# Optimization experiments

Hardware: AMD Instinct MI355X
Metric: run time of the kernel (lower is better)

The kernel has to match this reference:

```python
import jax, jax.numpy as jnp
import numpy as np

B, S, D, H = 2, 4096, 128, 128
EPS = 1e-6
NEG_INF = -1e30


def _complex_linear(xr, xi, Wr, Wi, br, bi):
    # x: (B,S,D); W: (H,D); complex linear (Wr + i Wi)(xr + i xi) + (br + i bi) per layer math:
    # real_out = (xr Wr + br) - (xi Wi + bi); imag_out = (xi Wr + br) + (xr Wi + bi)
    out_r = xr @ Wr.T + br - (xi @ Wi.T + bi)
    out_i = xi @ Wr.T + br + (xr @ Wi.T + bi)
    return out_r, out_i


def setup_inputs() -> dict:
    key = jax.random.key(0)
    ks = jax.random.split(key, 24)
    scale = 1.0 / np.sqrt(D)
    def W(k):
        return jax.random.normal(k, (H, D), jnp.float32) * scale
    def b(k):
        return jax.random.normal(k, (H,), jnp.float32) * 0.01
    inp = {
        "Z_q": jax.random.normal(ks[0], (B, 2, S, D, 1), jnp.float32),
        "Z_k": jax.random.normal(ks[1], (B, 2, S, D, 1), jnp.float32),
        "Z_v": jax.random.normal(ks[2], (B, 2, S, D, 1), jnp.float32),
        "Wq_r": W(ks[3]), "Wq_i": W(ks[4]), "bq_r": b(ks[5]), "bq_i": b(ks[6]),
        "Wk_r": W(ks[7]), "Wk_i": W(ks[8]), "bk_r": b(ks[9]), "bk_i": b(ks[10]),
        "Wv_r": W(ks[11]), "Wv_i": W(ks[12]), "bv_r": b(ks[13]), "bv_i": b(ks[14]),
        "Wp_r": W(ks[15]), "Wp_i": W(ks[16]), "bp_r": b(ks[17]), "bp_i": b(ks[18]),
        "noise_floor": jnp.asarray(1.0, jnp.float32),
        "tau": jnp.asarray(0.0, jnp.float32),
    }
    return inp


def reference(Z_q, Z_k, Z_v,
              Wq_r, Wq_i, bq_r, bq_i,
              Wk_r, Wk_i, bk_r, bk_i,
              Wv_r, Wv_i, bv_r, bv_i,
              Wp_r, Wp_i, bp_r, bp_i,
              noise_floor, tau):
    # squeeze trailing singleton; split real/imag -> (B,S,D)
    zqr, zqi = Z_q[:, 0, :, :, 0], Z_q[:, 1, :, :, 0]
    zkr, zki = Z_k[:, 0, :, :, 0], Z_k[:, 1, :, :, 0]
    zvr, zvi = Z_v[:, 0, :, :, 0], Z_v[:, 1, :, :, 0]

    Qr, Qi = _complex_linear(zqr, zqi, Wq_r, Wq_i, bq_r, bq_i)
    Kr, Ki = _complex_linear(zkr, zki, Wk_r, Wk_i, bk_r, bk_i)
    Vr, Vi = _complex_linear(zvr, zvi, Wv_r, Wv_i, bv_r, bv_i)

    # InverseMahalanobis: R2[b,i,j] = sum_h |Q[b,i]-K[b,j]|^2
    q2 = jnp.sum(Qr * Qr + Qi * Qi, axis=-1)          # (B,S)
    k2 = jnp.sum(Kr * Kr + Ki * Ki, axis=-1)          # (B,S)
    re_qk = (jnp.einsum('bsh,bth->bst', Qr, Kr)
             + jnp.einsum('bsh,bth->bst', Qi, Ki))    # (B,S,S)
    R2 = q2[:, :, None] + k2[:, None, :] - 2.0 * re_qk

    attn_scores = -jax.nn.softplus(tau) * jnp.log(noise_floor ** 2 + R2 + EPS)
    mask = jnp.tril(jnp.ones((S, S), dtype=bool))[None]
    attn_scores = jnp.where(mask, attn_scores, NEG_INF)
    attn_weights = jax.nn.softmax(attn_scores / jnp.sqrt(jnp.float32(H)), axis=-1)

    # attn (real) times complex V
    est_r = jnp.einsum('bst,bth->bsh', attn_weights, Vr)
    est_i = jnp.einsum('bst,bth->bsh', attn_weights, Vi)

    out_r, out_i = _complex_linear(est_r, est_i, Wp_r, Wp_i, bp_r, bp_i)
    out = jnp.stack((out_r, out_i), axis=1)[..., None]  # (B,2,S,H,1)
    return out, attn_weights
```

## Files before the change

### kernel.cpp

```cpp
#include <hip/hip_runtime.h>

#define S_LEN 4096
#define NBATCH 2
#define ROWS (NBATCH*S_LEN)
#define OUT_ELEMS 2097152

typedef _Float16 f16;
typedef _Float16 f16x8 __attribute__((ext_vector_type(8)));
typedef _Float16 f16x4 __attribute__((ext_vector_type(4)));
typedef float f32x4 __attribute__((ext_vector_type(4)));

#define MT_OFF    0x000000
#define BIAS_OFF  0x080000
#define SC_OFF    0x081000
#define QH_OFF    0x100000
#define KH_OFF    0x500000
#define VT_OFF    0x900000
#define Q2_OFF    0xD00000
#define K2_OFF    0xD10000
#define L_OFF     0xD20000
#define RS_OFF    0xE00000
#define EST_OFF   0x1200000
#define PW_OFF    0x9200000
#define WS_NEED   0xD200000

#define MFMA16(A,B,C) __builtin_amdgcn_mfma_f32_16x16x32_f16(A,B,C,0,0,0)

__device__ __forceinline__ void async_cp16(f16* lds, const f16* g) {
  __builtin_amdgcn_global_load_lds(
      (const __attribute__((address_space(1))) void*)g,
      (__attribute__((address_space(3))) void*)lds, 16, 0, 0);
}

template<int TR>
__device__ __forceinline__ void stage16(f16* lds, const f16* g, int stride, int tid) {
#pragma unroll
  for (int i = 0; i < TR/64; ++i) {
    int idx = i*256 + tid;
    int row = idx >> 2;
    int c = (idx & 3) ^ ((row >> 1) & 3);
    async_cp16(lds + idx*8, g + (size_t)row*stride + c*8);
  }
}

template<int TR>
__device__ __forceinline__ void stage32(f16* lds, const float* g, int stride, int tid,
                                        const float* rowscale) {
#pragma unroll
  for (int i = 0; i < TR/32; ++i) {
    int idx = i*256 + tid;
    int row = idx >> 3, c = idx & 7;
    const float4* gp = (const float4*)(g + (size_t)row*stride + c*4);
    float4 v = *gp;
    float sc = rowscale ? rowscale[row] : 1.0f;
    f16x4 h; h[0]=(f16)(v.x*sc); h[1]=(f16)(v.y*sc); h[2]=(f16)(v.z*sc); h[3]=(f16)(v.w*sc);
    int slot = (((c >> 1) ^ ((row >> 1) & 3)) << 3) + (c & 1)*4;
    *(f16x4*)(lds + row*32 + slot) = h;
  }
}

template<int MI, int NJ>
__device__ __forceinline__ void mfma_step(const f16* Asm, const f16* Bsm, int lane,
                                          int wm, int wn, f32x4 (&acc)[MI][NJ]) {
  f16x8 a[MI], b[NJ];
  int rr = lane & 15, kc = lane >> 4;
#pragma unroll
  for (int i=0;i<MI;i++) {
    int m = wm + i*16 + rr;
    a[i] = *(const f16x8*)(Asm + m*32 + ((kc ^ ((m>>1)&3)) << 3));
  }
#pragma unroll
  for (int j=0;j<NJ;j++) {
    int n = wn + j*16 + rr;
    b[j] = *(const f16x8*)(Bsm + n*32 + ((kc ^ ((n>>1)&3)) << 3));
  }
#pragma unroll
  for (int i=0;i<MI;i++)
#pragma unroll
    for (int j=0;j<NJ;j++) acc[i][j] = MFMA16(a[i], b[j], acc[i][j]);
}

__global__ __launch_bounds__(256)
void k_build(const float* Wqr, const float* Wqi, const float* bqr, const float* bqi,
             const float* Wkr, const float* Wki, const float* bkr, const float* bki,
             const float* Wvr, const float* Wvi, const float* bvr, const float* bvi,
             const float* Wpr, const float* Wpi, const float* bpr, const float* bpi,
             f16* Mt, float* bias) {
  int mat = blockIdx.x;
  const float *Wr, *Wi, *br, *bi;
  if (mat == 0)      { Wr=Wqr; Wi=Wqi; br=bqr; bi=bqi; }
  else if (mat == 1) { Wr=Wkr; Wi=Wki; br=bkr; bi=bki; }
  else if (mat == 2) { Wr=Wvr; Wi=Wvi; br=bvr; bi=bvi; }
  else               { Wr=Wpr; Wi=Wpi; br=bpr; bi=bpi; }
  int idx = blockIdx.y*256 + threadIdx.x;
  int n = idx >> 8, k = idx & 255;
  int d = k & 127, h = n & 127;
  float w = (k < 128) ? ((n < 128) ? Wr[h*128+d] : Wi[h*128+d])
                      : ((n < 128) ? -Wi[h*128+d] : Wr[h*128+d]);
  Mt[mat*65536 + n*256 + k] = (f16)w;
  if (k == 0)
    bias[mat*256 + n] = (n < 128) ? (br[n] - bi[n]) : (br[n-128] + bi[n-128]);
}

__global__ __launch_bounds__(256)
void k_init(float* zreg, float* sc, const float* nf, const float* tau) {
  int idx = blockIdx.x*256 + threadIdx.x;
  if (idx < 12288) ((float4*)zreg)[idx] = make_float4(0.f,0.f,0.f,0.f);
  if (idx == 0) {
    float t = tau[0];
    float c = __builtin_log2f(1.0f + __builtin_exp2f(t * 1.4426950408889634f))
              * 0.6931471805599453f;
    sc[0] = -c * 0.08838834764831845f;
    sc[1] = nf[0]*nf[0] + 1e-6f;
  }
}

__global__ __launch_bounds__(256)
void k_proj(const float* Zq, const float* Zk, const float* Zv,
            const f16* Mt, const float* bias,
            f16* Qh, f16* Kh, f16* Vt, float* q2, float* k2) {
  __shared__ f16 Asm[64*32];
  __shared__ f16 Bsm[128*32];
  __shared__ float bias_s[128];
  int tid = threadIdx.x;
  int mode = blockIdx.z;
  int m0 = blockIdx.x * 64, n0 = blockIdx.y * 128;
  const float* Z = (mode==0) ? Zq : (mode==1 ? Zk : Zv);
  const f16* Bt = Mt + mode*65536;
  if (tid < 128) bias_s[tid] = bias[mode*256 + n0 + tid];
  int b = m0 >> 12, s0 = m0 & 4095;
  int lane = tid & 63, w = tid >> 6;
  int wm = (w >> 1)*32, wn = (w & 1)*64;
  f32x4 acc[2][4] = {};
  for (int kb = 0; kb < 8; ++kb) {
    int k0 = kb*32;
    int part = k0 >> 7, d0 = k0 & 127;
    const float* Ag = Z + (((size_t)(b*2 + part))*S_LEN + s0)*128 + d0;
    stage32<64>(Asm, Ag, 128, tid, nullptr);
    stage16<128>(Bsm, Bt + n0*256 + k0, 256, tid);
    __syncthreads();
    mfma_step<2,4>(Asm, Bsm, lane, wm, wn, acc);
    __syncthreads();
  }
  int rr = (lane>>4)*4, cc = lane & 15;
  if (mode < 2) {
    f16* O = (mode==0) ? Qh : Kh;
    float rs[2][4];
#pragma unroll
    for (int i=0;i<2;i++)
#pragma unroll
      for (int r=0;r<4;r++) rs[i][r]=0.f;
#pragma unroll
    for (int i=0;i<2;i++)
#pragma unroll
      for (int j=0;j<4;j++) {
        int cl = wn + j*16 + cc;
        int cg = n0 + cl;
        float bv = bias_s[cl];
#pragma unroll
        for (int r=0;r<4;r++) {
          int rg = m0 + wm + i*16 + rr + r;
          f16 hv = (f16)(acc[i][j][r] + bv);
          O[(size_t)rg*256 + cg] = hv;
          float fv = (float)hv;
          rs[i][r] += fv*fv;
        }
      }
#pragma unroll
    for (int m=8;m>=1;m>>=1)
#pragma unroll
      for (int i=0;i<2;i++)
#pragma unroll
        for (int r=0;r<4;r++) rs[i][r] += __shfl_xor(rs[i][r], m, 64);
    if (cc == 0) {
      float* T = (mode==0) ? q2 : k2;
#pragma unroll
      for (int i=0;i<2;i++)
#pragma unroll
        for (int r=0;r<4;r++) {
          int rg = m0 + wm + i*16 + rr + r;
          atomicAdd(&T[rg], rs[i][r]);
        }
    }
  } else {
#pragma unroll
    for (int i=0;i<2;i++) {
      int t0 = s0 + wm + i*16 + rr;
#pragma unroll
      for (int j=0;j<4;j++) {
        int cl = wn + j*16 + cc;
        int cg = n0 + cl;
        float bv = bias_s[cl];
        f16x4 h4;
#pragma unroll
        for (int r=0;r<4;r++) h4[r] = (f16)(acc[i][j][r] + bv);
        *(f16x4*)(Vt + (size_t)b*1048576 + (size_t)cg*4096 + t0) = h4;
      }
    }
  }
}

__global__ __launch_bounds__(256)
void k_attn(const f16* Qh, const f16* Kh, const float* q2, const float* k2,
            const float* sc, float* rsum, f16* Pws) {
  __shared__ f16 Asm[128*32];
  __shared__ f16 Bsm[128*32];
  __shared__ float q2s[128], k2s[128];
  int x = blockIdx.x;
  int b = x / 528, r = x % 528;
  int sb = (int)((__builtin_sqrtf(8.f*(float)r + 1.f) - 1.f)*0.5f);
  while ((sb+1)*(sb+2)/2 <= r) sb++;
  while (sb*(sb+1)/2 > r) sb--;
  int tb = r - sb*(sb+1)/2;
  int s0 = sb*128, t0 = tb*128;
  int tid = threadIdx.x;
  if (tid < 128) {
    q2s[tid] = q2[b*S_LEN + s0 + tid];
    k2s[tid] = k2[b*S_LEN + t0 + tid];
  }
  float kc = sc[0], nf2 = sc[1];
  int lane = tid & 63, w = tid >> 6;
  int wm = (w >> 1)*64, wn = (w & 1)*64;
  const f16* Ag = Qh + ((size_t)(b*S_LEN) + s0)*256;
  const f16* Bg = Kh + ((size_t)(b*S_LEN) + t0)*256;
  f32x4 acc[4][4] = {};
  for (int kb=0;kb<8;kb++) {
    stage16<128>(Asm, Ag + kb*32, 256, tid);
    stage16<128>(Bsm, Bg + kb*32, 256, tid);
    __syncthreads();
    mfma_step<4,4>(Asm, Bsm, lane, wm, wn, acc);
    __syncthreads();
  }
  int rr = (lane>>4)*4, cc = lane & 15;
  bool diag = (tb == sb);
  float rs[4][4];
#pragma unroll
  for (int i=0;i<4;i++)
#pragma unroll
    for (int rg=0;rg<4;rg++) rs[i][rg]=0.f;
#pragma unroll
  for (int i=0;i<4;i++)
#pragma unroll
    for (int j=0;j<4;j++) {
      int cl = wn + j*16 + cc;
      float kv = k2s[cl];
#pragma unroll
      for (int rg=0;rg<4;rg++) {
        int rl = wm + i*16 + rr + rg;
        float xx = nf2 + q2s[rl] + kv - 2.0f*acc[i][j][rg];
        float P = __builtin_exp2f(kc * __builtin_log2f(__builtin_fmaxf(xx, 1e-6f)));
        if (diag && (t0+cl) > (s0+rl)) P = 0.f;
        Pws[((size_t)(b*S_LEN) + s0 + rl)*S_LEN + t0 + cl] = (f16)P;
        rs[i][rg] += P;
      }
    }
#pragma unroll
  for (int m=8;m>=1;m>>=1)
#pragma unroll
    for (int i=0;i<4;i++)
#pragma unroll
      for (int rg=0;rg<4;rg++) rs[i][rg] += __shfl_xor(rs[i][rg], m, 64);
  if (cc == 0) {
    float* R = rsum + ((size_t)((b*32+sb)*32+tb))*256 + (wn>>6)*128;
#pragma unroll
    for (int i=0;i<4;i++)
#pragma unroll
      for (int rg=0;rg<4;rg++)
        R[wm + i*16 + rr + rg] = rs[i][rg];
  }
}

__global__ __launch_bounds__(256)
void k_lred(const float* rsum, float* lsum) {
  int s = blockIdx.x*256 + threadIdx.x;
  int b = s >> 12, srow = s & 4095;
  int sb = srow >> 7, rowin = srow & 127;
  const float* R = rsum + ((size_t)((b*32+sb)*32))*256 + rowin;
  float acc = 0.f;
  for (int tb = 0; tb <= sb; ++tb) acc += R[tb*256] + R[tb*256+128];
  lsum[s] = acc;
}

__global__ __launch_bounds__(256)
void k_pv(const f16* Pws, const f16* Vt, float* est) {
  __shared__ f16 Asm[128*32];
  __shared__ f16 Bsm[128*32];
  int r = blockIdx.x;
  int nb = blockIdx.y, b = blockIdx.z;
  int sb = 0;
  while (r >= ((sb>>1)+1)) { r -= (sb>>1)+1; sb++; }
  int c = r;
  int s0 = sb*128, h0 = nb*128;
  int tid = threadIdx.x;
  int lane = tid & 63, w = tid >> 6;
  int wm = (w>>1)*64, wn = (w&1)*64;
  int tb0 = c*2, tb1 = tb0 + 2; if (tb1 > sb+1) tb1 = sb+1;
  const f16* Abase = Pws + ((size_t)(b*S_LEN) + s0)*S_LEN;
  const f16* Bbase = Vt + (size_t)b*1048576 + (size_t)h0*4096;
  f32x4 acc[4][4] = {};
  for (int tb = tb0; tb < tb1; ++tb)
    for (int kk = 0; kk < 4; ++kk) {
      int t0 = tb*128 + kk*32;
      stage16<128>(Asm, Abase + t0, S_LEN, tid);
      stage16<128>(Bsm, Bbase + t0, 4096, tid);
      __syncthreads();
      mfma_step<4,4>(Asm, Bsm, lane, wm, wn, acc);
      __syncthreads();
    }
  float* E = est + (size_t)c*2097152;
  int rr = (lane>>4)*4, cc = lane & 15;
#pragma unroll
  for (int i=0;i<4;i++)
#pragma unroll
    for (int j=0;j<4;j++) {
      int cg = h0 + wn + j*16 + cc;
#pragma unroll
      for (int rg=0;rg<4;rg++) {
        int rgl = s0 + wm + i*16 + rr + rg;
        E[((size_t)(b*S_LEN) + rgl)*256 + cg] = acc[i][j][rg];
      }
    }
}

__global__ __launch_bounds__(256)
void k_norm(const f16* __restrict__ Pws, const float* __restrict__ lsum,
            float* __restrict__ attn) {
  int base = blockIdx.x*1024 + threadIdx.x;
#pragma unroll
  for (int u = 0; u < 4; ++u) {
    int lin = base + u*256;
    int row = lin >> 10, t4 = lin & 1023;
    int srow = row & 4095;
    int t0 = t4 << 2;
    float4 o = make_float4(0.f,0.f,0.f,0.f);
    if (t0 <= srow) {
      float invl = 1.0f / lsum[row];
      f16x4 p = *(const f16x4*)(Pws + ((size_t)row<<12) + t0);
      o.x = (float)p[0]*invl;
      o.y = (t0+1 <= srow) ? (float)p[1]*invl : 0.f;
      o.z = (t0+2 <= srow) ? (float)p[2]*invl : 0.f;
      o.w = (t0+3 <= srow) ? (float)p[3]*invl : 0.f;
    }
    ((float4*)attn)[lin] = o;
  }
}

__global__ __launch_bounds__(256)
void k_out(const float* est, const f16* Mt, const float* bias, const float* lsum,
           float* outp) {
  __shared__ f16 Asm[16*32];
  __shared__ f16 Bsm[256*32];
  __shared__ float bias_s[256];
  __shared__ float ls[16];
  int m0 = blockIdx.x*16;
  int tid = threadIdx.x;
  int b = m0 >> 12, s0 = m0 & 4095;
  int sb = s0 >> 7, nch = (sb>>1) + 1;
  if (tid < 256) bias_s[tid] = bias[3*256 + tid];
  if (tid < 16)  ls[tid] = 1.0f / lsum[b*S_LEN + s0 + tid];
  __syncthreads();
  int lane = tid & 63, w = tid >> 6;
  int wn = w*64;
  const f16* Bt = Mt + 3*65536;
  f32x4 acc[1][4] = {};
  for (int kb=0;kb<8;kb++) {
    if (tid < 128) {
      int row = tid >> 3, c4 = tid & 7;
      const float* basep = est + ((size_t)(b*S_LEN) + s0 + row)*256 + kb*32 + c4*4;
      float4 v = make_float4(0.f,0.f,0.f,0.f);
      for (int ch = 0; ch < nch; ++ch) {
        float4 q = *(const float4*)(basep + (size_t)ch*2097152);
        v.x += q.x; v.y += q.y; v.z += q.z; v.w += q.w;
      }
      float scl = ls[row];
      f16x4 h; h[0]=(f16)(v.x*scl); h[1]=(f16)(v.y*scl); h[2]=(f16)(v.z*scl); h[3]=(f16)(v.w*scl);
      int slot = (((c4 >> 1) ^ ((row >> 1) & 3)) << 3) + (c4 & 1)*4;
      *(f16x4*)(Asm + row*32 + slot) = h;
    }
    stage16<256>(Bsm, Bt + kb*32, 256, tid);
    __syncthreads();
    mfma_step<1,4>(Asm, Bsm, lane, 0, wn, acc);
    __syncthreads();
  }
  int rr = (lane>>4)*4, cc = lane & 15;
#pragma unroll
  for (int j=0;j<4;j++) {
    int cg = wn + j*16 + cc;
    int comp = cg >> 7, h = cg & 127;
    float bv = bias_s[cg];
#pragma unroll
    for (int rg=0;rg<4;rg++) {
      int s = s0 + rr + rg;
      outp[(((size_t)(b*2 + comp))*S_LEN + s)*128 + h] = acc[0][j][rg] + bv;
    }
  }
}

extern "C" void kernel_launch(void* const* d_in, const int* in_sizes, int n_in,
                              void* d_out, int out_size, void* d_ws, size_t ws_size,
                              hipStream_t stream) {
  (void)in_sizes; (void)n_in; (void)out_size;
  if (ws_size < (size_t)WS_NEED) return;
  const float* Zq = (const float*)d_in[0];
  const float* Zk = (const float*)d_in[1];
  const float* Zv = (const float*)d_in[2];
  char* ws = (char*)d_ws;
  f16*   Mt   = (f16*)(ws + MT_OFF);
  float* bias = (float*)(ws + BIAS_OFF);
  float* sc   = (float*)(ws + SC_OFF);
  f16*   Qh   = (f16*)(ws + QH_OFF);
  f16*   Kh   = (f16*)(ws + KH_OFF);
  f16*   Vt   = (f16*)(ws + VT_OFF);
  float* q2   = (float*)(ws + Q2_OFF);
  float* k2   = (float*)(ws + K2_OFF);
  float* lsum = (float*)(ws + L_OFF);
  float* rsum = (float*)(ws + RS_OFF);
  float* est  = (float*)(ws + EST_OFF);
  f16*   Pws  = (f16*)(ws + PW_OFF);
  float* outp = (float*)d_out;
  float* attn = outp + OUT_ELEMS;

  k_build<<<dim3(4,256), 256, 0, stream>>>(
      (const float*)d_in[3],  (const float*)d_in[4],  (const float*)d_in[5],  (const float*)d_in[6],
      (const float*)d_in[7],  (const float*)d_in[8],  (const float*)d_in[9],  (const float*)d_in[10],
      (const float*)d_in[11], (const float*)d_in[12], (const float*)d_in[13], (const float*)d_in[14],
      (const float*)d_in[15], (const float*)d_in[16], (const float*)d_in[17], (const float*)d_in[18],
      Mt, bias);
  k_init<<<48, 256, 0, stream>>>(q2, sc, (const float*)d_in[19], (const float*)d_in[20]);
  k_proj<<<dim3(128,2,3), 256, 0, stream>>>(Zq, Zk, Zv, Mt, bias, Qh, Kh, Vt, q2, k2);
  k_attn<<<1056, 256, 0, stream>>>(Qh, Kh, q2, k2, sc, rsum, Pws);
  k_lred<<<32, 256, 0, stream>>>(rsum, lsum);
  k_pv<<<dim3(272,2,2), 256, 0, stream>>>(Pws, Vt, est);
  k_norm<<<8192, 256, 0, stream>>>(Pws, lsum, attn);
  k_out<<<512, 256, 0, stream>>>(est, Mt, bias, lsum, outp);
}
```

Before: 355.4 us.

## Fuse pipeline into persistent megakernel with grid barriers and balanced PV split

Replaces the separate projection, attention, row-sum, PV, normalization and output kernels with one persistent 512-block kernel that moves between phases through software grid barriers. PV work is redistributed into four balanced splits per row-block pair with partial outputs zeroed up front. Atomics for q2/k2 are replaced with partial sums written per slice. This removes launch gaps and load imbalance, but relies on all 512 blocks being co-resident for the barrier, and the normalize and output phases now share the grid.

```diff
diff --git a/kernel.cpp b/kernel.cpp
--- a/kernel.cpp
+++ b/kernel.cpp
@@ -4,6 +4,7 @@
 #define NBATCH 2
 #define ROWS (NBATCH*S_LEN)
 #define OUT_ELEMS 2097152
+#define NBLK 512
 
 typedef _Float16 f16;
 typedef _Float16 f16x8 __attribute__((ext_vector_type(8)));
@@ -13,16 +14,17 @@
 #define MT_OFF    0x000000
 #define BIAS_OFF  0x080000
 #define SC_OFF    0x081000
+#define BAR_OFF   0x082000
 #define QH_OFF    0x100000
 #define KH_OFF    0x500000
 #define VT_OFF    0x900000
-#define Q2_OFF    0xD00000
-#define K2_OFF    0xD10000
-#define L_OFF     0xD20000
+#define Q2P_OFF   0xD00000
+#define K2P_OFF   0xD20000
+#define LS_OFF    0xD40000
 #define RS_OFF    0xE00000
-#define EST_OFF   0x1200000
-#define PW_OFF    0x9200000
-#define WS_NEED   0xD200000
+#define ESTP_OFF  0x1200000
+#define PW_OFF    0x3200000
+#define WS_NEED   0x7200000
 
 #define MFMA16(A,B,C) __builtin_amdgcn_mfma_f32_16x16x32_f16(A,B,C,0,0,0)
 
@@ -44,16 +46,14 @@
 }
 
 template<int TR>
-__device__ __forceinline__ void stage32(f16* lds, const float* g, int stride, int tid,
-                                        const float* rowscale) {
+__device__ __forceinline__ void stage32(f16* lds, const float* g, int stride, int tid) {
 #pragma unroll
   for (int i = 0; i < TR/32; ++i) {
     int idx = i*256 + tid;
     int row = idx >> 3, c = idx & 7;
     const float4* gp = (const float4*)(g + (size_t)row*stride + c*4);
     float4 v = *gp;
-    float sc = rowscale ? rowscale[row] : 1.0f;
-    f16x4 h; h[0]=(f16)(v.x*sc); h[1]=(f16)(v.y*sc); h[2]=(f16)(v.z*sc); h[3]=(f16)(v.w*sc);
+    f16x4 h; h[0]=(f16)v.x; h[1]=(f16)v.y; h[2]=(f16)v.z; h[3]=(f16)v.w;
     int slot = (((c >> 1) ^ ((row >> 1) & 3)) << 3) + (c & 1)*4;
     *(f16x4*)(lds + row*32 + slot) = h;
   }
@@ -80,318 +80,355 @@
     for (int j=0;j<NJ;j++) acc[i][j] = MFMA16(a[i], b[j], acc[i][j]);
 }
 
+__device__ __forceinline__ void gbar(int* bar) {
+  __syncthreads();
+  if (threadIdx.x == 0) {
+    __threadfence();
+    int gen = __hip_atomic_load(&bar[1], __ATOMIC_RELAXED, __HIP_MEMORY_SCOPE_AGENT);
+    int old = __hip_atomic_fetch_add(&bar[0], 1, __ATOMIC_ACQ_REL, __HIP_MEMORY_SCOPE_AGENT);
+    if (old == NBLK-1) {
+      __hip_atomic_store(&bar[0], 0, __ATOMIC_RELAXED, __HIP_MEMORY_SCOPE_AGENT);
+      __hip_atomic_fetch_add(&bar[1], 1, __ATOMIC_RELEASE, __HIP_MEMORY_SCOPE_AGENT);
+    } else {
+      while (__hip_atomic_load(&bar[1], __ATOMIC_ACQUIRE, __HIP_MEMORY_SCOPE_AGENT) == gen)
+        __builtin_amdgcn_s_sleep(2);
+    }
+    __threadfence();
+  }
+  __syncthreads();
+}
+
 __global__ __launch_bounds__(256)
-void k_build(const float* Wqr, const float* Wqi, const float* bqr, const float* bqi,
-             const float* Wkr, const float* Wki, const float* bkr, const float* bki,
-             const float* Wvr, const float* Wvi, const float* bvr, const float* bvi,
-             const float* Wpr, const float* Wpi, const float* bpr, const float* bpi,
-             f16* Mt, float* bias) {
-  int mat = blockIdx.x;
-  const float *Wr, *Wi, *br, *bi;
-  if (mat == 0)      { Wr=Wqr; Wi=Wqi; br=bqr; bi=bqi; }
-  else if (mat == 1) { Wr=Wkr; Wi=Wki; br=bkr; bi=bki; }
-  else if (mat == 2) { Wr=Wvr; Wi=Wvi; br=bvr; bi=bvi; }
-  else               { Wr=Wpr; Wi=Wpi; br=bpr; bi=bpi; }
-  int idx = blockIdx.y*256 + threadIdx.x;
-  int n = idx >> 8, k = idx & 255;
-  int d = k & 127, h = n & 127;
-  float w = (k < 128) ? ((n < 128) ? Wr[h*128+d] : Wi[h*128+d])
-                      : ((n < 128) ? -Wi[h*128+d] : Wr[h*128+d]);
-  Mt[mat*65536 + n*256 + k] = (f16)w;
-  if (k == 0)
-    bias[mat*256 + n] = (n < 128) ? (br[n] - bi[n]) : (br[n-128] + bi[n-128]);
-}
-
-__global__ __launch_bounds__(256)
-void k_init(float* zreg, float* sc, const float* nf, const float* tau) {
+void k_init(const float* Wqr, const float* Wqi, const float* bqr, const float* bqi,
+            const float* Wkr, const float* Wki, const float* bkr, const float* bki,
+            const float* Wvr, const float* Wvi, const float* bvr, const float* bvi,
+            const float* Wpr, const float* Wpi, const float* bpr, const float* bpi,
+            f16* Mt, float* bias, float* sc, float* estp, int* bar,
+            const float* nf, const float* tau) {
   int idx = blockIdx.x*256 + threadIdx.x;
-  if (idx < 12288) ((float4*)zreg)[idx] = make_float4(0.f,0.f,0.f,0.f);
+  if (idx < 262144) {
+    int mat = idx >> 16, rest = idx & 65535;
+    int n = rest >> 8, k = rest & 255;
+    const float *Wr, *Wi, *br, *bi;
+    if (mat == 0)      { Wr=Wqr; Wi=Wqi; br=bqr; bi=bqi; }
+    else if (mat == 1) { Wr=Wkr; Wi=Wki; br=bkr; bi=bki; }
+    else if (mat == 2) { Wr=Wvr; Wi=Wvi; br=bvr; bi=bvi; }
+    else               { Wr=Wpr; Wi=Wpi; br=bpr; bi=bpi; }
+    int d = k & 127, h = n & 127;
+    float w = (k < 128) ? ((n < 128) ? Wr[h*128+d] : Wi[h*128+d])
+                        : ((n < 128) ? -Wi[h*128+d] : Wr[h*128+d]);
+    Mt[mat*65536 + n*256 + k] = (f16)w;
+    if (k == 0)
+      bias[mat*256 + n] = (n < 128) ? (br[n] - bi[n]) : (br[n-128] + bi[n-128]);
+  }
+  float4 z = make_float4(0.f,0.f,0.f,0.f);
+#pragma unroll
+  for (int u = 0; u < 4; ++u)
+    ((float4*)estp)[idx + u*524288] = z;
   if (idx == 0) {
     float t = tau[0];
     float c = __builtin_log2f(1.0f + __builtin_exp2f(t * 1.4426950408889634f))
               * 0.6931471805599453f;
     sc[0] = -c * 0.08838834764831845f;
     sc[1] = nf[0]*nf[0] + 1e-6f;
-  }
-}
-
-__global__ __launch_bounds__(256)
-void k_proj(const float* Zq, const float* Zk, const float* Zv,
-            const f16* Mt, const float* bias,
-            f16* Qh, f16* Kh, f16* Vt, float* q2, float* k2) {
-  __shared__ f16 Asm[64*32];
-  __shared__ f16 Bsm[128*32];
-  __shared__ float bias_s[128];
-  int tid = threadIdx.x;
-  int mode = blockIdx.z;
-  int m0 = blockIdx.x * 64, n0 = blockIdx.y * 128;
-  const float* Z = (mode==0) ? Zq : (mode==1 ? Zk : Zv);
-  const f16* Bt = Mt + mode*65536;
-  if (tid < 128) bias_s[tid] = bias[mode*256 + n0 + tid];
-  int b = m0 >> 12, s0 = m0 & 4095;
+    bar[0] = 0; bar[1] = 0;
+  }
+}
+
+__global__ __launch_bounds__(256, 2)
+void k_mega(const float* Zq, const float* Zk, const float* Zv,
+            const f16* Mt, const float* bias, const float* sc,
+            f16* Qh, f16* Kh, f16* Vt, float* q2p, float* k2p,
+            float* rsum, float* lsum, float* estp, f16* Pws,
+            float* attn, float* outp, int* bar) {
+  __shared__ __align__(16) char smem[18496];
+  int bid = blockIdx.x, tid = threadIdx.x;
   int lane = tid & 63, w = tid >> 6;
-  int wm = (w >> 1)*32, wn = (w & 1)*64;
-  f32x4 acc[2][4] = {};
-  for (int kb = 0; kb < 8; ++kb) {
-    int k0 = kb*32;
-    int part = k0 >> 7, d0 = k0 & 127;
-    const float* Ag = Z + (((size_t)(b*2 + part))*S_LEN + s0)*128 + d0;
-    stage32<64>(Asm, Ag, 128, tid, nullptr);
-    stage16<128>(Bsm, Bt + n0*256 + k0, 256, tid);
+  int rr = (lane>>4)*4, cc = lane & 15;
+
+  for (int job = bid; job < 768; job += NBLK) {
+    f16* Asm = (f16*)smem;
+    f16* Bsm = (f16*)(smem + 4096);
+    float* bias_s = (float*)(smem + 12288);
+    int mode = job >> 8, rem = job & 255;
+    int m0 = (rem >> 1)*64, n0 = (rem & 1)*128;
+    const float* Z = (mode==0) ? Zq : (mode==1 ? Zk : Zv);
+    const f16* Bt = Mt + mode*65536;
+    if (tid < 128) bias_s[tid] = bias[mode*256 + n0 + tid];
+    int b = m0 >> 12, s0 = m0 & 4095;
+    int wm = (w >> 1)*32, wn = (w & 1)*64;
+    f32x4 acc[2][4] = {};
+    for (int kb = 0; kb < 8; ++kb) {
+      int k0 = kb*32;
+      int part = k0 >> 7, d0 = k0 & 127;
+      const float* Ag = Z + (((size_t)(b*2 + part))*S_LEN + s0)*128 + d0;
+      stage32<64>(Asm, Ag, 128, tid);
+      stage16<128>(Bsm, Bt + n0*256 + k0, 256, tid);
+      __syncthreads();
+      mfma_step<2,4>(Asm, Bsm, lane, wm, wn, acc);
+      __syncthreads();
+    }
+    if (mode < 2) {
+      f16* O = (mode==0) ? Qh : Kh;
+      float rs[2][4];
+#pragma unroll
+      for (int i=0;i<2;i++)
+#pragma unroll
+        for (int r=0;r<4;r++) rs[i][r]=0.f;
+#pragma unroll
+      for (int i=0;i<2;i++)
+#pragma unroll
+        for (int j=0;j<4;j++) {
+          int cl = wn + j*16 + cc;
+          float bv = bias_s[cl];
+#pragma unroll
+          for (int r=0;r<4;r++) {
+            int rg = m0 + wm + i*16 + rr + r;
+            f16 hv = (f16)(acc[i][j][r] + bv);
+            O[(size_t)rg*256 + n0 + cl] = hv;
+            float fv = (float)hv;
+            rs[i][r] += fv*fv;
+          }
+        }
+#pragma unroll
+      for (int m=8;m>=1;m>>=1)
+#pragma unroll
+        for (int i=0;i<2;i++)
+#pragma unroll
+          for (int r=0;r<4;r++) rs[i][r] += __shfl_xor(rs[i][r], m, 64);
+      if (cc == 0) {
+        float* T = ((mode==0) ? q2p : k2p) + ((n0>>7)*2 + (wn>>6))*8192;
+#pragma unroll
+        for (int i=0;i<2;i++)
+#pragma unroll
+          for (int r=0;r<4;r++)
+            T[m0 + wm + i*16 + rr + r] = rs[i][r];
+      }
+    } else {
+#pragma unroll
+      for (int i=0;i<2;i++) {
+        int t0 = s0 + wm + i*16 + rr;
+#pragma unroll
+        for (int j=0;j<4;j++) {
+          int cl = wn + j*16 + cc;
+          float bv = bias_s[cl];
+          f16x4 h4;
+#pragma unroll
+          for (int r=0;r<4;r++) h4[r] = (f16)(acc[i][j][r] + bv);
+          *(f16x4*)(Vt + (size_t)b*1048576 + (size_t)(n0+cl)*4096 + t0) = h4;
+        }
+      }
+    }
     __syncthreads();
-    mfma_step<2,4>(Asm, Bsm, lane, wm, wn, acc);
-    __syncthreads();
-  }
-  int rr = (lane>>4)*4, cc = lane & 15;
-  if (mode < 2) {
-    f16* O = (mode==0) ? Qh : Kh;
-    float rs[2][4];
-#pragma unroll
-    for (int i=0;i<2;i++)
-#pragma unroll
-      for (int r=0;r<4;r++) rs[i][r]=0.f;
-#pragma unroll
-    for (int i=0;i<2;i++)
+  }
+  gbar(bar);
+
+  for (int job = bid; job < 1056; job += NBLK) {
+    f16* Asm = (f16*)smem;
+    f16* Bsm = (f16*)(smem + 8192);
+    float* q2s = (float*)(smem + 16384);
+    float* k2s = (float*)(smem + 16896);
+    int b = job / 528, r = job % 528;
+    int sb = (int)((__builtin_sqrtf(8.f*(float)r + 1.f) - 1.f)*0.5f);
+    while ((sb+1)*(sb+2)/2 <= r) sb++;
+    while (sb*(sb+1)/2 > r) sb--;
+    int tb = r - sb*(sb+1)/2;
+    int s0 = sb*128, t0 = tb*128;
+    if (tid < 128) {
+      int rq = b*S_LEN + s0 + tid, rk = b*S_LEN + t0 + tid;
+      q2s[tid] = q2p[rq] + q2p[8192+rq] + q2p[16384+rq] + q2p[24576+rq];
+      k2s[tid] = k2p[rk] + k2p[8192+rk] + k2p[16384+rk] + k2p[24576+rk];
+    }
+    float kcs = sc[0], nf2 = sc[1];
+    int wm = (w >> 1)*64, wn = (w & 1)*64;
+    const f16* Ag = Qh + ((size_t)(b*S_LEN) + s0)*256;
+    const f16* Bg = Kh + ((size_t)(b*S_LEN) + t0)*256;
+    f32x4 acc[4][4] = {};
+    for (int kb=0;kb<8;kb++) {
+      stage16<128>(Asm, Ag + kb*32, 256, tid);
+      stage16<128>(Bsm, Bg + kb*32, 256, tid);
+      __syncthreads();
+      mfma_step<4,4>(Asm, Bsm, lane, wm, wn, acc);
+      __syncthreads();
+    }
+    bool diag = (tb == sb);
+    float rs[4][4];
+#pragma unroll
+    for (int i=0;i<4;i++)
+#pragma unroll
+      for (int rg=0;rg<4;rg++) rs[i][rg]=0.f;
+#pragma unroll
+    for (int i=0;i<4;i++)
 #pragma unroll
       for (int j=0;j<4;j++) {
         int cl = wn + j*16 + cc;
-        int cg = n0 + cl;
-        float bv = bias_s[cl];
-#pragma unroll
-        for (int r=0;r<4;r++) {
-          int rg = m0 + wm + i*16 + rr + r;
-          f16 hv = (f16)(acc[i][j][r] + bv);
-          O[(size_t)rg*256 + cg] = hv;
-          float fv = (float)hv;
-          rs[i][r] += fv*fv;
+        float kv = k2s[cl];
+#pragma unroll
+        for (int rg=0;rg<4;rg++) {
+          int rl = wm + i*16 + rr + rg;
+          float xx = nf2 + q2s[rl] + kv - 2.0f*acc[i][j][rg];
+          float P = __builtin_exp2f(kcs * __builtin_log2f(__builtin_fmaxf(xx, 1e-6f)));
+          if (diag && (t0+cl) > (s0+rl)) P = 0.f;
+          Pws[((size_t)(b*S_LEN) + s0 + rl)*S_LEN + t0 + cl] = (f16)P;
+          rs[i][rg] += P;
         }
       }
 #pragma unroll
     for (int m=8;m>=1;m>>=1)
 #pragma unroll
-      for (int i=0;i<2;i++)
-#pragma unroll
-        for (int r=0;r<4;r++) rs[i][r] += __shfl_xor(rs[i][r], m, 64);
+      for (int i=0;i<4;i++)
+#pragma unroll
+        for (int rg=0;rg<4;rg++) rs[i][rg] += __shfl_xor(rs[i][rg], m, 64);
     if (cc == 0) {
-      float* T = (mode==0) ? q2 : k2;
-#pragma unroll
-      for (int i=0;i<2;i++)
-#pragma unroll
-        for (int r=0;r<4;r++) {
-          int rg = m0 + wm + i*16 + rr + r;
-          atomicAdd(&T[rg], rs[i][r]);
-        }
+      float* R = rsum + ((size_t)((b*32+sb)*32+tb))*256 + (wn>>6)*128;
+#pragma unroll
+      for (int i=0;i<4;i++)
+#pragma unroll
+        for (int rg=0;rg<4;rg++)
+          R[wm + i*16 + rr + rg] = rs[i][rg];
+    }
+    __syncthreads();
+  }
+  gbar(bar);
+
+  if (bid < 256) {
+    f16* Asm = (f16*)smem;
+    f16* Bsm = (f16*)(smem + 8192);
+    int j = bid;
+    int p = j & 15, spl = (j>>4)&3, nbh = (j>>6)&1, b = j>>7;
+    int h0 = nbh*128;
+    int wm = (w>>1)*64, wn = (w&1)*64;
+    int st = (33*spl + 3) >> 2;
+    int en = (33*spl + 36) >> 2;
+    const f16* Bbase = Vt + (size_t)b*1048576 + (size_t)h0*4096;
+    f32x4 acc[4][4] = {};
+    int currow = -1;
+    for (int idx = st; idx < en; ++idx) {
+      int row = (idx <= p) ? p : 31-p;
+      int tb  = (idx <= p) ? idx : idx - (p+1);
+      if (row != currow) {
+        if (currow >= 0) {
+          float* E = estp + (size_t)spl*2097152 + ((size_t)(b*S_LEN) + currow*128)*256;
+#pragma unroll
+          for (int i=0;i<4;i++)
+#pragma unroll
+            for (int j2=0;j2<4;j2++)
+#pragma unroll
+              for (int rg=0;rg<4;rg++) {
+                E[(size_t)(wm + i*16 + rr + rg)*256 + h0 + wn + j2*16 + cc] = acc[i][j2][rg];
+                acc[i][j2][rg] = 0.f;
+              }
+        }
+        currow = row;
+      }
+      const f16* Abase = Pws + ((size_t)(b*S_LEN) + row*128)*S_LEN;
+      for (int kk=0;kk<4;kk++) {
+        int t0 = tb*128 + kk*32;
+        stage16<128>(Asm, Abase + t0, S_LEN, tid);
+        stage16<128>(Bsm, Bbase + t0, 4096, tid);
+        __syncthreads();
+        mfma_step<4,4>(Asm, Bsm, lane, wm, wn, acc);
+        __syncthreads();
+      }
+    }
+    {
+      float* E = estp + (size_t)spl*2097152 + ((size_t)(b*S_LEN) + currow*128)*256;
+#pragma unroll
+      for (int i=0;i<4;i++)
+#pragma unroll
+        for (int j2=0;j2<4;j2++)
+#pragma unroll
+          for (int rg=0;rg<4;rg++)
+            E[(size_t)(wm + i*16 + rr + rg)*256 + h0 + wn + j2*16 + cc] = acc[i][j2][rg];
     }
   } else {
-#pragma unroll
-    for (int i=0;i<2;i++) {
-      int t0 = s0 + wm + i*16 + rr;
-#pragma unroll
-      for (int j=0;j<4;j++) {
-        int cl = wn + j*16 + cc;
-        int cg = n0 + cl;
-        float bv = bias_s[cl];
-        f16x4 h4;
-#pragma unroll
-        for (int r=0;r<4;r++) h4[r] = (f16)(acc[i][j][r] + bv);
-        *(f16x4*)(Vt + (size_t)b*1048576 + (size_t)cg*4096 + t0) = h4;
-      }
-    }
-  }
-}
-
-__global__ __launch_bounds__(256)
-void k_attn(const f16* Qh, const f16* Kh, const float* q2, const float* k2,
-            const float* sc, float* rsum, f16* Pws) {
-  __shared__ f16 Asm[128*32];
-  __shared__ f16 Bsm[128*32];
-  __shared__ float q2s[128], k2s[128];
-  int x = blockIdx.x;
-  int b = x / 528, r = x % 528;
-  int sb = (int)((__builtin_sqrtf(8.f*(float)r + 1.f) - 1.f)*0.5f);
-  while ((sb+1)*(sb+2)/2 <= r) sb++;
-  while (sb*(sb+1)/2 > r) sb--;
-  int tb = r - sb*(sb+1)/2;
-  int s0 = sb*128, t0 = tb*128;
-  int tid = threadIdx.x;
-  if (tid < 128) {
-    q2s[tid] = q2[b*S_LEN + s0 + tid];
-    k2s[tid] = k2[b*S_LEN + t0 + tid];
-  }
-  float kc = sc[0], nf2 = sc[1];
-  int lane = tid & 63, w = tid >> 6;
-  int wm = (w >> 1)*64, wn = (w & 1)*64;
-  const f16* Ag = Qh + ((size_t)(b*S_LEN) + s0)*256;
-  const f16* Bg = Kh + ((size_t)(b*S_LEN) + t0)*256;
-  f32x4 acc[4][4] = {};
-  for (int kb=0;kb<8;kb++) {
-    stage16<128>(Asm, Ag + kb*32, 256, tid);
-    stage16<128>(Bsm, Bg + kb*32, 256, tid);
+    float* part = (float*)smem;
+    float* lss  = (float*)(smem + 1024);
+    int nb2 = bid - 256;
+    {
+      int r2 = tid >> 3, j8 = tid & 7;
+      int rowg = nb2*32 + r2;
+      int b = rowg >> 12, srow = rowg & 4095;
+      int sb = srow >> 7, rowin = srow & 127;
+      const float* R = rsum + ((size_t)((b*32+sb)*32))*256 + rowin;
+      float s = 0.f;
+      for (int tb = j8; tb <= sb; tb += 8) s += R[tb*256] + R[tb*256+128];
+      part[tid] = s;
+    }
     __syncthreads();
-    mfma_step<4,4>(Asm, Bsm, lane, wm, wn, acc);
+    if (tid < 32) {
+      float s = 0.f;
+#pragma unroll
+      for (int u=0;u<8;u++) s += part[tid*8+u];
+      lss[tid] = s;
+      lsum[nb2*32 + tid] = s;
+    }
     __syncthreads();
-  }
-  int rr = (lane>>4)*4, cc = lane & 15;
-  bool diag = (tb == sb);
-  float rs[4][4];
-#pragma unroll
-  for (int i=0;i<4;i++)
-#pragma unroll
-    for (int rg=0;rg<4;rg++) rs[i][rg]=0.f;
-#pragma unroll
-  for (int i=0;i<4;i++)
+    for (int r2 = 0; r2 < 32; ++r2) {
+      int rowg = nb2*32 + r2;
+      int srow = rowg & 4095;
+      float invl = 1.0f / lss[r2];
+      const f16* src = Pws + (size_t)rowg*S_LEN;
+      float4* dst = (float4*)(attn + (size_t)rowg*S_LEN);
+      for (int q = tid; q < 1024; q += 256) {
+        int t0 = q*4;
+        float4 o = make_float4(0.f,0.f,0.f,0.f);
+        if (t0 <= srow) {
+          f16x4 pv4 = *(const f16x4*)(src + t0);
+          o.x = (float)pv4[0]*invl;
+          o.y = (t0+1 <= srow) ? (float)pv4[1]*invl : 0.f;
+          o.z = (t0+2 <= srow) ? (float)pv4[2]*invl : 0.f;
+          o.w = (t0+3 <= srow) ? (float)pv4[3]*invl : 0.f;
+        }
+        dst[q] = o;
+      }
+    }
+  }
+  gbar(bar);
+
+  {
+    f16* Asm = (f16*)smem;
+    f16* Bsm = (f16*)(smem + 1024);
+    float* bias_s = (float*)(smem + 1024 + 16384);
+    float* ls = (float*)(smem + 1024 + 16384 + 1024);
+    int m0 = bid*16;
+    int b = m0 >> 12, s0 = m0 & 4095;
+    bias_s[tid] = bias[3*256 + tid];
+    if (tid < 16) ls[tid] = 1.0f / lsum[b*S_LEN + s0 + tid];
+    __syncthreads();
+    int wn = w*64;
+    const f16* Bt = Mt + 3*65536;
+    f32x4 acc[1][4] = {};
+    for (int kb=0;kb<8;kb++) {
+      if (tid < 128) {
+        int row = tid >> 3, c4 = tid & 7;
+        const float* basep = estp + ((size_t)(b*S_LEN) + s0 + row)*256 + kb*32 + c4*4;
+        float4 v = make_float4(0.f,0.f,0.f,0.f);
+#pragma unroll
+        for (int ch = 0; ch < 4; ++ch) {
+          float4 q = *(const float4*)(basep + (size_t)ch*2097152);
+          v.x += q.x; v.y += q.y; v.z += q.z; v.w += q.w;
+        }
+        float scl = ls[row];
+        f16x4 h; h[0]=(f16)(v.x*scl); h[1]=(f16)(v.y*scl); h[2]=(f16)(v.z*scl); h[3]=(f16)(v.w*scl);
+        int slot = (((c4 >> 1) ^ ((row >> 1) & 3)) << 3) + (c4 & 1)*4;
+        *(f16x4*)(Asm + row*32 + slot) = h;
+      }
+      stage16<256>(Bsm, Bt + kb*32, 256, tid);
+      __syncthreads();
+      mfma_step<1,4>(Asm, Bsm, lane, 0, wn, acc);
+      __syncthreads();
+    }
 #pragma unroll
     for (int j=0;j<4;j++) {
-      int cl = wn + j*16 + cc;
-      float kv = k2s[cl];
+      int cg = wn + j*16 + cc;
+      int comp = cg >> 7, h = cg & 127;
+      float bv = bias_s[cg];
 #pragma unroll
       for (int rg=0;rg<4;rg++) {
-        int rl = wm + i*16 + rr + rg;
-        float xx = nf2 + q2s[rl] + kv - 2.0f*acc[i][j][rg];
-        float P = __builtin_exp2f(kc * __builtin_log2f(__builtin_fmaxf(xx, 1e-6f)));
-        if (diag && (t0+cl) > (s0+rl)) P = 0.f;
-        Pws[((size_t)(b*S_LEN) + s0 + rl)*S_LEN + t0 + cl] = (f16)P;
-        rs[i][rg] += P;
-      }
-    }
-#pragma unroll
-  for (int m=8;m>=1;m>>=1)
-#pragma unroll
-    for (int i=0;i<4;i++)
-#pragma unroll
-      for (int rg=0;rg<4;rg++) rs[i][rg] += __shfl_xor(rs[i][rg], m, 64);
-  if (cc == 0) {
-    float* R = rsum + ((size_t)((b*32+sb)*32+tb))*256 + (wn>>6)*128;
-#pragma unroll
-    for (int i=0;i<4;i++)
-#pragma unroll
-      for (int rg=0;rg<4;rg++)
-        R[wm + i*16 + rr + rg] = rs[i][rg];
-  }
-}
-
-__global__ __launch_bounds__(256)
-void k_lred(const float* rsum, float* lsum) {
-  int s = blockIdx.x*256 + threadIdx.x;
-  int b = s >> 12, srow = s & 4095;
-  int sb = srow >> 7, rowin = srow & 127;
-  const float* R = rsum + ((size_t)((b*32+sb)*32))*256 + rowin;
-  float acc = 0.f;
-  for (int tb = 0; tb <= sb; ++tb) acc += R[tb*256] + R[tb*256+128];
-  lsum[s] = acc;
-}
-
-__global__ __launch_bounds__(256)
-void k_pv(const f16* Pws, const f16* Vt, float* est) {
-  __shared__ f16 Asm[128*32];
-  __shared__ f16 Bsm[128*32];
-  int r = blockIdx.x;
-  int nb = blockIdx.y, b = blockIdx.z;
-  int sb = 0;
-  while (r >= ((sb>>1)+1)) { r -= (sb>>1)+1; sb++; }
-  int c = r;
-  int s0 = sb*128, h0 = nb*128;
-  int tid = threadIdx.x;
-  int lane = tid & 63, w = tid >> 6;
-  int wm = (w>>1)*64, wn = (w&1)*64;
-  int tb0 = c*2, tb1 = tb0 + 2; if (tb1 > sb+1) tb1 = sb+1;
-  const f16* Abase = Pws + ((size_t)(b*S_LEN) + s0)*S_LEN;
-  const f16* Bbase = Vt + (size_t)b*1048576 + (size_t)h0*4096;
-  f32x4 acc[4][4] = {};
-  for (int tb = tb0; tb < tb1; ++tb)
-    for (int kk = 0; kk < 4; ++kk) {
-      int t0 = tb*128 + kk*32;
-      stage16<128>(Asm, Abase + t0, S_LEN, tid);
-      stage16<128>(Bsm, Bbase + t0, 4096, tid);
-      __syncthreads();
-      mfma_step<4,4>(Asm, Bsm, lane, wm, wn, acc);
-      __syncthreads();
-    }
-  float* E = est + (size_t)c*2097152;
-  int rr = (lane>>4)*4, cc = lane & 15;
-#pragma unroll
-  for (int i=0;i<4;i++)
-#pragma unroll
-    for (int j=0;j<4;j++) {
-      int cg = h0 + wn + j*16 + cc;
-#pragma unroll
-      for (int rg=0;rg<4;rg++) {
-        int rgl = s0 + wm + i*16 + rr + rg;
-        E[((size_t)(b*S_LEN) + rgl)*256 + cg] = acc[i][j][rg];
-      }
-    }
-}
-
-__global__ __launch_bounds__(256)
-void k_norm(const f16* __restrict__ Pws, const float* __restrict__ lsum,
-            float* __restrict__ attn) {
-  int base = blockIdx.x*1024 + threadIdx.x;
-#pragma unroll
-  for (int u = 0; u < 4; ++u) {
-    int lin = base + u*256;
-    int row = lin >> 10, t4 = lin & 1023;
-    int srow = row & 4095;
-    int t0 = t4 << 2;
-    float4 o = make_float4(0.f,0.f,0.f,0.f);
-    if (t0 <= srow) {
-      float invl = 1.0f / lsum[row];
-      f16x4 p = *(const f16x4*)(Pws + ((size_t)row<<12) + t0);
-      o.x = (float)p[0]*invl;
-      o.y = (t0+1 <= srow) ? (float)p[1]*invl : 0.f;
-      o.z = (t0+2 <= srow) ? (float)p[2]*invl : 0.f;
-      o.w = (t0+3 <= srow) ? (float)p[3]*invl : 0.f;
-    }
-    ((float4*)attn)[lin] = o;
-  }
-}
-
-__global__ __launch_bounds__(256)
-void k_out(const float* est, const f16* Mt, const float* bias, const float* lsum,
-           float* outp) {
-  __shared__ f16 Asm[16*32];
-  __shared__ f16 Bsm[256*32];
-  __shared__ float bias_s[256];
-  __shared__ float ls[16];
-  int m0 = blockIdx.x*16;
-  int tid = threadIdx.x;
-  int b = m0 >> 12, s0 = m0 & 4095;
-  int sb = s0 >> 7, nch = (sb>>1) + 1;
-  if (tid < 256) bias_s[tid] = bias[3*256 + tid];
-  if (tid < 16)  ls[tid] = 1.0f / lsum[b*S_LEN + s0 + tid];
-  __syncthreads();
-  int lane = tid & 63, w = tid >> 6;
-  int wn = w*64;
-  const f16* Bt = Mt + 3*65536;
-  f32x4 acc[1][4] = {};
-  for (int kb=0;kb<8;kb++) {
-    if (tid < 128) {
-      int row = tid >> 3, c4 = tid & 7;
-      const float* basep = est + ((size_t)(b*S_LEN) + s0 + row)*256 + kb*32 + c4*4;
-      float4 v = make_float4(0.f,0.f,0.f,0.f);
-      for (int ch = 0; ch < nch; ++ch) {
-        float4 q = *(const float4*)(basep + (size_t)ch*2097152);
-        v.x += q.x; v.y += q.y; v.z += q.z; v.w += q.w;
-      }
-      float scl = ls[row];
-      f16x4 h; h[0]=(f16)(v.x*scl); h[1]=(f16)(v.y*scl); h[2]=(f16)(v.z*scl); h[3]=(f16)(v.w*scl);
-      int slot = (((c4 >> 1) ^ ((row >> 1) & 3)) << 3) + (c4 & 1)*4;
-      *(f16x4*)(Asm + row*32 + slot) = h;
-    }
-    stage16<256>(Bsm, Bt + kb*32, 256, tid);
-    __syncthreads();
-    mfma_step<1,4>(Asm, Bsm, lane, 0, wn, acc);
-    __syncthreads();
-  }
-  int rr = (lane>>4)*4, cc = lane & 15;
-#pragma unroll
-  for (int j=0;j<4;j++) {
-    int cg = wn + j*16 + cc;
-    int comp = cg >> 7, h = cg & 127;
-    float bv = bias_s[cg];
-#pragma unroll
-    for (int rg=0;rg<4;rg++) {
-      int s = s0 + rr + rg;
-      outp[(((size_t)(b*2 + comp))*S_LEN + s)*128 + h] = acc[0][j][rg] + bv;
+        int s = s0 + rr + rg;
+        outp[(((size_t)(b*2 + comp))*S_LEN + s)*128 + h] = acc[0][j][rg] + bv;
+      }
     }
   }
 }
@@ -401,36 +438,30 @@
                               hipStream_t stream) {
   (void)in_sizes; (void)n_in; (void)out_size;
   if (ws_size < (size_t)WS_NEED) return;
-  const float* Zq = (const float*)d_in[0];
-  const float* Zk = (const float*)d_in[1];
-  const float* Zv = (const float*)d_in[2];
   char* ws = (char*)d_ws;
   f16*   Mt   = (f16*)(ws + MT_OFF);
   float* bias = (float*)(ws + BIAS_OFF);
   float* sc   = (float*)(ws + SC_OFF);
+  int*   bar  = (int*)(ws + BAR_OFF);
   f16*   Qh   = (f16*)(ws + QH_OFF);
   f16*   Kh   = (f16*)(ws + KH_OFF);
   f16*   Vt   = (f16*)(ws + VT_OFF);
-  float* q2   = (float*)(ws + Q2_OFF);
-  float* k2   = (float*)(ws + K2_OFF);
-  float* lsum = (float*)(ws + L_OFF);
+  float* q2p  = (float*)(ws + Q2P_OFF);
+  float* k2p  = (float*)(ws + K2P_OFF);
+  float* lsum = (float*)(ws + LS_OFF);
   float* rsum = (float*)(ws + RS_OFF);
-  float* est  = (float*)(ws + EST_OFF);
+  float* estp = (float*)(ws + ESTP_OFF);
   f16*   Pws  = (f16*)(ws + PW_OFF);
   float* outp = (float*)d_out;
   float* attn = outp + OUT_ELEMS;
 
-  k_build<<<dim3(4,256), 256, 0, stream>>>(
+  k_init<<<2048, 256, 0, stream>>>(
       (const float*)d_in[3],  (const float*)d_in[4],  (const float*)d_in[5],  (const float*)d_in[6],
       (const float*)d_in[7],  (const float*)d_in[8],  (const float*)d_in[9],  (const float*)d_in[10],
       (const float*)d_in[11], (const float*)d_in[12], (const float*)d_in[13], (const float*)d_in[14],
       (const float*)d_in[15], (const float*)d_in[16], (const float*)d_in[17], (const float*)d_in[18],
-      Mt, bias);
-  k_init<<<48, 256, 0, stream>>>(q2, sc, (const float*)d_in[19], (const float*)d_in[20]);
-  k_proj<<<dim3(128,2,3), 256, 0, stream>>>(Zq, Zk, Zv, Mt, bias, Qh, Kh, Vt, q2, k2);
-  k_attn<<<1056, 256, 0, stream>>>(Qh, Kh, q2, k2, sc, rsum, Pws);
-  k_lred<<<32, 256, 0, stream>>>(rsum, lsum);
-  k_pv<<<dim3(272,2,2), 256, 0, stream>>>(Pws, Vt, est);
-  k_norm<<<8192, 256, 0, stream>>>(Pws, lsum, attn);
-  k_out<<<512, 256, 0, stream>>>(est, Mt, bias, lsum, outp);
-}
+      Mt, bias, sc, estp, bar, (const float*)d_in[19], (const float*)d_in[20]);
+  k_mega<<<NBLK, 256, 0, stream>>>(
+      (const float*)d_in[0], (const float*)d_in[1], (const float*)d_in[2],
+      Mt, bias, sc, Qh, Kh, Vt, q2p, k2p, rsum, lsum, estp, Pws, attn, outp, bar);
+}
```

New measurement: 807.8 us. 2.27x slower.
